# Kernel tuning notes

Hardware: AMD Instinct MI355X
Metric: run time of the kernel (lower is better)

## Reference

```python
import jax, jax.numpy as jnp
import numpy as np
from functools import partial

DN = ('NCHW', 'OIHW', 'NCHW')

def conv2d(x, w, b, stride):
    y = jax.lax.conv_general_dilated(x, w, (stride, stride), 'VALID', dimension_numbers=DN)
    return y + b[None, :, None, None]

def squash(s, eps=1e-8):
    norm = jnp.linalg.norm(s, axis=-1, keepdims=True)
    return (norm ** 2 / (1 + norm ** 2)) * s / (norm + eps)

def setup_inputs() -> dict:
    key = jax.random.key(0)
    ks = jax.random.split(key, 10)
    B, H, W = 16, 32, 512
    F, CAPS, E, OD = 64, 8, 8, 16
    H1 = (H - 6) // 2 + 1          # 14
    W1 = (W - 6) // 2 + 1          # 254
    N = F * H1 * W1 // CAPS        # 28448
    s = 0.05
    return {
        'x': jax.random.normal(ks[0], (B, H, W), jnp.float32),
        'conv1_w': jax.random.normal(ks[1], (F, 1, 6, 6), jnp.float32) * s,
        'conv1_b': jnp.zeros((F,), jnp.float32),
        'conv2_w': jax.random.normal(ks[2], (F, F, 6, 6), jnp.float32) * s,
        'conv2_b': jnp.zeros((F,), jnp.float32),
        'conv3_w': jax.random.normal(ks[3], (F, 2 * F, 1, 1), jnp.float32) * s,
        'conv3_b': jnp.zeros((F,), jnp.float32),
        'pc_w': jax.random.normal(ks[4], (N, CAPS, CAPS), jnp.float32) * s,  # [N, in, out]
        'pc_b': jnp.zeros((N, CAPS), jnp.float32),
        'ec_w': jax.random.normal(ks[5], (N, E, OD, CAPS), jnp.float32),
    }

def reference(x, conv1_w, conv1_b, conv2_w, conv2_b, conv3_w, conv3_b, pc_w, pc_b, ec_w):
    CAPS = pc_w.shape[1]
    NUM_ITER = 3
    B = x.shape[0]
    h = x[:, None]                                  # [B,1,H,W]
    h = jax.nn.relu(conv2d(h, conv1_w, conv1_b, 2)) # [B,F,14,254]
    y = jnp.pad(h, ((0, 0), (0, 0), (2, 3), (2, 3)))  # ZeroPad2d((2,3,2,3))
    y = jax.nn.relu(conv2d(y, conv2_w, conv2_b, 1))
    h = jax.nn.relu(jnp.concatenate((h, y), axis=1))
    h = conv2d(h, conv3_w, conv3_b, 1)              # [B,F,14,254]
    u_in = h.reshape(B, -1, CAPS)                   # [B,N,caps_len]
    # PrimaryCaps: N independent Linear(caps,caps) -> one batched einsum
    u = jnp.einsum('bni,nio->bno', u_in, pc_w) + pc_b[None]
    # EmotionCaps: per-capsule prediction u_hat [B,N,E,out_dim]
    u_hat = jnp.einsum('neoi,bni->bneo', ec_w, u)
    N, E = ec_w.shape[0], ec_w.shape[1]
    b_log = jnp.zeros((B, N, E), u_hat.dtype)
    v = None
    for r in range(NUM_ITER):
        c = jax.nn.softmax(b_log, axis=2)           # [B,N,E]
        s = jnp.einsum('bne,bneo->beo', c, u_hat)   # [B,E,out_dim]
        v = squash(s)
        if r < NUM_ITER - 1:
            b_log = b_log + jnp.einsum('bneo,beo->bne', u_hat, v)
    return jnp.linalg.norm(v, axis=-1)              # [B,E]
```

## Files before the change

### kernel.cpp

```cpp
#include <hip/hip_runtime.h>
#include <hip/hip_bf16.h>
#include <math.h>

#define BB 16
#define H1 14
#define W1 254
#define HPH 19
#define HPW2 264
#define NCAP 28448
#define FLATSZ 227584

typedef __attribute__((ext_vector_type(8))) short bf16x8;
typedef __attribute__((ext_vector_type(4))) float f32x4;

__device__ __forceinline__ ushort f2bf(float f) {
  __hip_bfloat16 h = __float2bfloat16(f);
  return *(ushort*)&h;
}

__global__ __launch_bounds__(256) void prep_w(const float* __restrict__ w2, const float* __restrict__ w3,
                                              ushort* __restrict__ wb, float* __restrict__ w3t) {
  int idx = blockIdx.x * 256 + threadIdx.x;
  if (idx < 147456) {
    int co = idx / 2304; int rem = idx - co * 2304;
    int tap = rem >> 6; int ci = rem & 63;
    wb[idx] = f2bf(w2[(co * 64 + ci) * 36 + tap]);
  }
  if (idx < 8192) {
    int co = idx & 63; int c = idx >> 6;
    w3t[idx] = w3[co * 128 + c];
  }
}

__global__ __launch_bounds__(256) void conv1_k(const float* __restrict__ x, const float* __restrict__ w1,
                                               const float* __restrict__ b1, float* __restrict__ hc) {
  const int i = blockIdx.x, b = blockIdx.y;
  __shared__ float xs[6 * 512];
  __shared__ float wsh[2304];
  __shared__ float bsh[64];
  const int t = threadIdx.x;
  for (int idx = t; idx < 6 * 512; idx += 256) {
    int r = idx >> 9, c = idx & 511;
    xs[idx] = x[((size_t)b * 32 + 2 * i + r) * 512 + c];
  }
  for (int idx = t; idx < 2304; idx += 256) wsh[idx] = w1[idx];
  if (t < 64) bsh[t] = b1[t];
  __syncthreads();
  if (t < 254) {
    for (int c = 0; c < 64; c++) {
      float acc = bsh[c];
#pragma unroll
      for (int p = 0; p < 6; p++)
#pragma unroll
        for (int q = 0; q < 6; q++)
          acc = fmaf(xs[p * 512 + 2 * t + q], wsh[c * 36 + p * 6 + q], acc);
      acc = fmaxf(acc, 0.f);
      hc[(((size_t)b * 64 + c) * H1 + i) * W1 + t] = acc;
    }
  }
}

__global__ __launch_bounds__(256) void nhwc_k(const float* __restrict__ hc, ushort* __restrict__ hpc) {
  const int ct = blockIdx.x, i = blockIdx.y, b = blockIdx.z;
  const int c0 = ct * 64;
  __shared__ float ls[64 * 65];
  const int t = threadIdx.x;
  for (int idx = t; idx < 4096; idx += 256) {
    int ci = idx >> 6, cc = idx & 63;
    int c = c0 + cc;
    ls[ci * 65 + cc] = (c < W1) ? hc[(((size_t)b * 64 + ci) * H1 + i) * W1 + c] : 0.f;
  }
  __syncthreads();
  uint* outp = (uint*)hpc;
  for (int idx = t; idx < 2048; idx += 256) {
    int cc = idx >> 5, ci2 = idx & 31;
    int c = c0 + cc;
    if (c < W1) {
      float f0 = ls[(2 * ci2) * 65 + cc];
      float f1 = ls[(2 * ci2 + 1) * 65 + cc];
      uint pk = (uint)f2bf(f0) | ((uint)f2bf(f1) << 16);
      outp[(((size_t)b * HPH + 2 + i) * HPW2 + 2 + c) * 32 + ci2] = pk;
    }
  }
}

__device__ __forceinline__ void stage_b(const ushort* __restrict__ wb, ushort* __restrict__ bbuf,
                                        int tap, int w, int l) {
#pragma unroll
  for (int r = 0; r < 2; r++) {
    int v = r * 256 + w * 64 + l;
    int co = v >> 3, s = v & 7;
    int g = s ^ (co & 7);
    const ushort* gp = wb + co * 2304 + tap * 64 + g * 8;
    ushort* lp = bbuf + (size_t)(r * 256 + w * 64) * 8;
    __builtin_amdgcn_global_load_lds((const uint*)gp, (uint*)lp, 16, 0, 0);
  }
}

__global__ __launch_bounds__(256, 1) void conv2_mfma(const ushort* __restrict__ hpc,
                                                     const ushort* __restrict__ wb,
                                                     const float* __restrict__ b2, float* __restrict__ y) {
  const int b = blockIdx.z, i = blockIdx.y, j0 = blockIdx.x * 128;
  const int t = threadIdx.x;
  const int w = t >> 6, l = t & 63;
  const int lr = l & 15, quad = l >> 4;

  __shared__ ushort bls[2][4096];

  f32x4 acc[2][4];
#pragma unroll
  for (int mt = 0; mt < 2; mt++)
#pragma unroll
    for (int nt = 0; nt < 4; nt++) acc[mt][nt] = (f32x4){0.f, 0.f, 0.f, 0.f};

  const ushort* abase = hpc + (((size_t)b * HPH + i) * HPW2 + (j0 + w * 32 + lr)) * 64 + quad * 8;

  bf16x8 a0[2][2], a1[2][2];

#define ALOAD(dst, tap)                                                        \
  {                                                                            \
    const int p_ = (tap) / 6, q_ = (tap) % 6;                                  \
    const ushort* ap_ = abase + ((size_t)p_ * HPW2 + q_) * 64;                 \
    dst[0][0] = *(const bf16x8*)(ap_);                                         \
    dst[0][1] = *(const bf16x8*)(ap_ + 1024);                                  \
    dst[1][0] = *(const bf16x8*)(ap_ + 32);                                    \
    dst[1][1] = *(const bf16x8*)(ap_ + 32 + 1024);                             \
  }

#define COMPUTE(a, bp)                                                         \
  {                                                                            \
    _Pragma("unroll")                                                          \
    for (int ch = 0; ch < 2; ch++) {                                           \
      const int g2 = ch * 4 + quad;                                            \
      _Pragma("unroll")                                                        \
      for (int nt = 0; nt < 4; nt++) {                                         \
        const int co = nt * 16 + lr;                                           \
        bf16x8 bf = *(const bf16x8*)((bp) + co * 64 + ((g2 ^ (co & 7)) * 8));  \
        acc[0][nt] = __builtin_amdgcn_mfma_f32_16x16x32_bf16(a[ch][0], bf, acc[0][nt], 0, 0, 0); \
        acc[1][nt] = __builtin_amdgcn_mfma_f32_16x16x32_bf16(a[ch][1], bf, acc[1][nt], 0, 0, 0); \
      }                                                                        \
    }                                                                          \
  }

  stage_b(wb, &bls[0][0], 0, w, l);
  __syncthreads();
  ALOAD(a0, 0);

  for (int tp = 0; tp < 36; tp += 2) {
    stage_b(wb, &bls[1][0], tp + 1, w, l);
    ALOAD(a1, tp + 1);
    COMPUTE(a0, &bls[0][0]);
    __syncthreads();
    if (tp + 2 < 36) {
      stage_b(wb, &bls[0][0], tp + 2, w, l);
      ALOAD(a0, tp + 2);
    }
    COMPUTE(a1, &bls[1][0]);
    __syncthreads();
  }

#pragma unroll
  for (int nt = 0; nt < 4; nt++) {
    const int co = nt * 16 + lr;
    const float bias = b2[co];
    float* yrow = y + (((size_t)b * 64 + co) * H1 + i) * W1;
#pragma unroll
    for (int mt = 0; mt < 2; mt++) {
      const int jb = j0 + w * 32 + mt * 16 + quad * 4;
#pragma unroll
      for (int r = 0; r < 4; r++) {
        int j = jb + r;
        if (j < W1) yrow[j] = fmaxf(acc[mt][nt][r] + bias, 0.f);
      }
    }
  }
#undef ALOAD
#undef COMPUTE
}

__global__ __launch_bounds__(256) void conv3_k(const float* __restrict__ hc, const float* __restrict__ y,
                                               const float* __restrict__ w3t, const float* __restrict__ b3,
                                               float* __restrict__ out3) {
  const int b = blockIdx.z, i = blockIdx.y, j0 = blockIdx.x * 64;
  __shared__ float cs[32][64];
  __shared__ float wsh[32][64];
  const int t = threadIdx.x;
  const int cog = t >> 4, jg = t & 15;
  float acc[4][4];
#pragma unroll
  for (int a = 0; a < 4; a++)
#pragma unroll
    for (int j = 0; j < 4; j++) acc[a][j] = 0.f;

  for (int ch = 0; ch < 4; ch++) {
    __syncthreads();
    for (int idx = t; idx < 2048; idx += 256) {
      int cl = idx >> 6; int j = j0 + (idx & 63);
      int c = ch * 32 + cl;
      float v = 0.f;
      if (j < W1) {
        if (c < 64) v = hc[(((size_t)b * 64 + c) * H1 + i) * W1 + j];
        else        v = y[(((size_t)b * 64 + (c - 64)) * H1 + i) * W1 + j];
      }
      cs[cl][idx & 63] = v;
    }
    for (int idx = t; idx < 2048; idx += 256)
      wsh[idx >> 6][idx & 63] = w3t[(ch * 32 + (idx >> 6)) * 64 + (idx & 63)];
    __syncthreads();
#pragma unroll
    for (int c = 0; c < 32; c++) {
      float4 xv = *(const float4*)&cs[c][jg * 4];
      float4 wv = *(const float4*)&wsh[c][cog * 4];
#pragma unroll
      for (int jj = 0; jj < 4; jj++) {
        float xx = (&xv.x)[jj];
        acc[0][jj] = fmaf(wv.x, xx, acc[0][jj]);
        acc[1][jj] = fmaf(wv.y, xx, acc[1][jj]);
        acc[2][jj] = fmaf(wv.z, xx, acc[2][jj]);
        acc[3][jj] = fmaf(wv.w, xx, acc[3][jj]);
      }
    }
  }
#pragma unroll
  for (int a = 0; a < 4; a++) {
    int co = cog * 4 + a;
    float bias = b3[co];
#pragma unroll
    for (int jj = 0; jj < 4; jj++) {
      int j = j0 + jg * 4 + jj;
      if (j < W1) out3[(((size_t)b * 64 + co) * H1 + i) * W1 + j] = acc[a][jj] + bias;
    }
  }
}

__global__ __launch_bounds__(256) void pc_k(const float* __restrict__ out3, const float* __restrict__ pcw,
                                            const float* __restrict__ pcb, float* __restrict__ u) {
  int n = blockIdx.x * 256 + threadIdx.x;
  if (n >= NCAP) return;
  float pw[64];
  const float4* pwp = (const float4*)(pcw + (size_t)n * 64);
#pragma unroll
  for (int k = 0; k < 16; k++) {
    float4 v = pwp[k];
    pw[4 * k] = v.x; pw[4 * k + 1] = v.y; pw[4 * k + 2] = v.z; pw[4 * k + 3] = v.w;
  }
  float pb[8];
  {
    const float4* pbp = (const float4*)(pcb + (size_t)n * 8);
    float4 a = pbp[0], b = pbp[1];
    pb[0] = a.x; pb[1] = a.y; pb[2] = a.z; pb[3] = a.w;
    pb[4] = b.x; pb[5] = b.y; pb[6] = b.z; pb[7] = b.w;
  }
  for (int b = 0; b < BB; b++) {
    const float4* uip = (const float4*)(out3 + (size_t)b * FLATSZ + (size_t)n * 8);
    float4 a = uip[0], c = uip[1];
    float ui[8] = {a.x, a.y, a.z, a.w, c.x, c.y, c.z, c.w};
    float uo[8];
#pragma unroll
    for (int o = 0; o < 8; o++) uo[o] = pb[o];
#pragma unroll
    for (int i2 = 0; i2 < 8; i2++)
#pragma unroll
      for (int o = 0; o < 8; o++) uo[o] = fmaf(ui[i2], pw[i2 * 8 + o], uo[o]);
    float4* up = (float4*)(u + ((size_t)b * NCAP + n) * 8);
    up[0] = make_float4(uo[0], uo[1], uo[2], uo[3]);
    up[1] = make_float4(uo[4], uo[5], uo[6], uo[7]);
  }
}

template <int MODE>
__global__ __launch_bounds__(256, 4) void route_k(const float* __restrict__ u, const float* __restrict__ ecw,
                                                  const float* __restrict__ v, float* __restrict__ sout) {
  const int t = threadIdx.x, l = t & 63, wv = t >> 6;
  const int b0 = blockIdx.y * 8;
  const int n0 = blockIdx.x * 32 + wv * 8;

  __shared__ float us[4][512];
  __shared__ float red[4096];
  __shared__ float vlds[1024];

  if (MODE) {
    for (int idx = t; idx < 1024; idx += 256) vlds[idx] = v[b0 * 128 + idx];
    __syncthreads();
  }

#pragma unroll
  for (int bb = 0; bb < 8; bb++)
    us[wv][bb * 64 + l] = u[((size_t)(b0 + bb) * NCAP + n0) * 8 + l];

  float sacc[16];
#pragma unroll
  for (int k = 0; k < 16; k++) sacc[k] = 0.f;

  for (int nn = 0; nn < 8; nn++) {
    const int n = n0 + nn;
    const float4* ep = (const float4*)(ecw + (size_t)n * 1024 + l * 16);
    float4 e0 = ep[0], e1 = ep[1], e2 = ep[2], e3 = ep[3];
    float ec[16] = {e0.x, e0.y, e0.z, e0.w, e1.x, e1.y, e1.z, e1.w,
                    e2.x, e2.y, e2.z, e2.w, e3.x, e3.y, e3.z, e3.w};
#pragma unroll
    for (int bb = 0; bb < 8; bb++) {
      const float4* up = (const float4*)&us[wv][bb * 64 + nn * 8];
      float4 ua = up[0], ubv = up[1];
      float uv[8] = {ua.x, ua.y, ua.z, ua.w, ubv.x, ubv.y, ubv.z, ubv.w};
      float h0 = 0.f, h1 = 0.f;
#pragma unroll
      for (int k = 0; k < 8; k++) { h0 = fmaf(ec[k], uv[k], h0); h1 = fmaf(ec[8 + k], uv[k], h1); }
      if (MODE == 0) {
        sacc[2 * bb] += h0; sacc[2 * bb + 1] += h1;
      } else {
        float2 vv = *(const float2*)&vlds[bb * 128 + 2 * l];
        float p = h0 * vv.x + h1 * vv.y;
        p += __shfl_xor(p, 1); p += __shfl_xor(p, 2); p += __shfl_xor(p, 4);
        float m = p;
        m = fmaxf(m, __shfl_xor(m, 8)); m = fmaxf(m, __shfl_xor(m, 16)); m = fmaxf(m, __shfl_xor(m, 32));
        float ex = __expf(p - m);
        float den = ex;
        den += __shfl_xor(den, 8); den += __shfl_xor(den, 16); den += __shfl_xor(den, 32);
        float cc = ex * __builtin_amdgcn_rcpf(den);
        sacc[2 * bb] = fmaf(cc, h0, sacc[2 * bb]);
        sacc[2 * bb + 1] = fmaf(cc, h1, sacc[2 * bb + 1]);
      }
    }
  }

#pragma unroll
  for (int k = 0; k < 16; k++) red[k * 256 + wv * 64 + l] = sacc[k];
  __syncthreads();
#pragma unroll
  for (int m = 0; m < 4; m++) {
    int slot = t + 256 * m;
    int bl = slot >> 7, eo = slot & 127;
    int k = 2 * bl + (eo & 1), l2 = eo >> 1;
    const float* r = red + k * 256 + l2;
    atomicAdd(&sout[(b0 + bl) * 128 + eo], r[0] + r[64] + r[128] + r[192]);
  }
}

__global__ void squash_k(const float* __restrict__ s, float scale, const float* __restrict__ vprev,
                         float* __restrict__ vout) {
  int t = threadIdx.x;
  const float* sp = s + t * 16;
  float sv[16]; float nn = 0.f;
#pragma unroll
  for (int o = 0; o < 16; o++) { float x = sp[o] * scale; sv[o] = x; nn = fmaf(x, x, nn); }
  float norm = sqrtf(nn);
  float f = nn / (1.f + nn) / (norm + 1e-8f);
#pragma unroll
  for (int o = 0; o < 16; o++) {
    float base = vprev ? vprev[t * 16 + o] : 0.f;
    vout[t * 16 + o] = base + f * sv[o];
  }
}

__global__ void squash_out_k(const float* __restrict__ s, float* __restrict__ out) {
  int t = threadIdx.x;
  float nn = 0.f;
#pragma unroll
  for (int o = 0; o < 16; o++) { float x = s[t * 16 + o]; nn = fmaf(x, x, nn); }
  float norm = sqrtf(nn);
  float f = nn / (1.f + nn) / (norm + 1e-8f);
  out[t] = f * norm;
}

extern "C" void kernel_launch(void* const* d_in, const int* in_sizes, int n_in,
                              void* d_out, int out_size, void* d_ws, size_t ws_size,
                              hipStream_t stream) {
  const float* x   = (const float*)d_in[0];
  const float* w1  = (const float*)d_in[1];
  const float* b1  = (const float*)d_in[2];
  const float* w2  = (const float*)d_in[3];
  const float* b2  = (const float*)d_in[4];
  const float* w3  = (const float*)d_in[5];
  const float* b3  = (const float*)d_in[6];
  const float* pcw = (const float*)d_in[7];
  const float* pcb = (const float*)d_in[8];
  const float* ecw = (const float*)d_in[9];
  float* out = (float*)d_out;

  float* ws = (float*)d_ws;
  size_t o = 0;
  float* hc   = ws + o; o += 3641344;
  float* yb   = ws + o; o += 3641344;
  float* out3 = ws + o; o += 3641344;
  ushort* hpc = (ushort*)(ws + o); o += 2568192;
  ushort* wb  = (ushort*)(ws + o); o += 73728;
  float* w3t  = ws + o; o += 8192;
  float* s0   = ws + o; o += 2048;
  float* s1   = ws + o; o += 2048;
  float* s2   = ws + o; o += 2048;
  float* v0   = ws + o; o += 2048;
  float* v1   = ws + o; o += 2048;
  float* ub   = hc;

  hipMemsetAsync(hpc, 0, (size_t)16 * HPH * HPW2 * 64 * 2, stream);
  hipMemsetAsync(s0, 0, 3 * 2048 * 4, stream);

  prep_w<<<576, 256, 0, stream>>>(w2, w3, wb, w3t);
  conv1_k<<<dim3(14, 16), 256, 0, stream>>>(x, w1, b1, hc);
  nhwc_k<<<dim3(4, 14, 16), 256, 0, stream>>>(hc, hpc);
  conv2_mfma<<<dim3(2, 14, 16), 256, 0, stream>>>(hpc, wb, b2, yb);
  conv3_k<<<dim3(4, 14, 16), 256, 0, stream>>>(hc, yb, w3t, b3, out3);
  pc_k<<<112, 256, 0, stream>>>(out3, pcw, pcb, ub);
  route_k<0><<<dim3(889, 2), 256, 0, stream>>>(ub, ecw, nullptr, s0);
  squash_k<<<1, 128, 0, stream>>>(s0, 0.125f, nullptr, v0);
  route_k<1><<<dim3(889, 2), 256, 0, stream>>>(ub, ecw, v0, s1);
  squash_k<<<1, 128, 0, stream>>>(s1, 1.0f, v0, v1);
  route_k<1><<<dim3(889, 2), 256, 0, stream>>>(ub, ecw, v1, s2);
  squash_out_k<<<1, 128, 0, stream>>>(s2, out);
}
```

Baseline: 495.6 us.

## Prefetch next capsule weights in routing kernel and drop softmax max reduction

The routing kernel now loads the ec_w row for the next capsule into registers while computing on the current one, so global loads overlap the arithmetic. The per-batch work is split into groups of four, which exposes more independent FMAs and shuffles at once. The softmax over emotions no longer subtracts the max, which removes three shuffle-max steps. The shared-memory barrier is also moved to after the u staging. Skipping the max trades numerical safety for fewer instructions, since large routing logits could overflow exp. The extra live registers may also reduce occupancy.

```diff
diff --git a/kernel.cpp b/kernel.cpp
--- a/kernel.cpp
+++ b/kernel.cpp
@@ -281,45 +281,67 @@
 
   if (MODE) {
     for (int idx = t; idx < 1024; idx += 256) vlds[idx] = v[b0 * 128 + idx];
-    __syncthreads();
-  }
-
+  }
 #pragma unroll
   for (int bb = 0; bb < 8; bb++)
     us[wv][bb * 64 + l] = u[((size_t)(b0 + bb) * NCAP + n0) * 8 + l];
+  if (MODE) __syncthreads();
 
   float sacc[16];
 #pragma unroll
   for (int k = 0; k < 16; k++) sacc[k] = 0.f;
 
+  const float4* ebase = (const float4*)(ecw + (size_t)n0 * 1024 + l * 16);
+
+  float eca[16];
+  {
+    float4 a = ebase[0], b = ebase[1], c = ebase[2], d = ebase[3];
+    eca[0]=a.x; eca[1]=a.y; eca[2]=a.z; eca[3]=a.w; eca[4]=b.x; eca[5]=b.y; eca[6]=b.z; eca[7]=b.w;
+    eca[8]=c.x; eca[9]=c.y; eca[10]=c.z; eca[11]=c.w; eca[12]=d.x; eca[13]=d.y; eca[14]=d.z; eca[15]=d.w;
+  }
+
   for (int nn = 0; nn < 8; nn++) {
-    const int n = n0 + nn;
-    const float4* ep = (const float4*)(ecw + (size_t)n * 1024 + l * 16);
-    float4 e0 = ep[0], e1 = ep[1], e2 = ep[2], e3 = ep[3];
-    float ec[16] = {e0.x, e0.y, e0.z, e0.w, e1.x, e1.y, e1.z, e1.w,
-                    e2.x, e2.y, e2.z, e2.w, e3.x, e3.y, e3.z, e3.w};
-#pragma unroll
-    for (int bb = 0; bb < 8; bb++) {
-      const float4* up = (const float4*)&us[wv][bb * 64 + nn * 8];
-      float4 ua = up[0], ubv = up[1];
-      float uv[8] = {ua.x, ua.y, ua.z, ua.w, ubv.x, ubv.y, ubv.z, ubv.w};
-      float h0 = 0.f, h1 = 0.f;
-#pragma unroll
-      for (int k = 0; k < 8; k++) { h0 = fmaf(ec[k], uv[k], h0); h1 = fmaf(ec[8 + k], uv[k], h1); }
+    float ec[16];
+#pragma unroll
+    for (int k = 0; k < 16; k++) ec[k] = eca[k];
+    if (nn < 7) {
+      const float4* ep = ebase + (nn + 1) * 256;
+      float4 a = ep[0], b = ep[1], c = ep[2], d = ep[3];
+      eca[0]=a.x; eca[1]=a.y; eca[2]=a.z; eca[3]=a.w; eca[4]=b.x; eca[5]=b.y; eca[6]=b.z; eca[7]=b.w;
+      eca[8]=c.x; eca[9]=c.y; eca[10]=c.z; eca[11]=c.w; eca[12]=d.x; eca[13]=d.y; eca[14]=d.z; eca[15]=d.w;
+    }
+#pragma unroll
+    for (int g = 0; g < 2; g++) {
+      float uh0[4], uh1[4];
+#pragma unroll
+      for (int j = 0; j < 4; j++) {
+        const float4* up = (const float4*)&us[wv][(g * 4 + j) * 64 + nn * 8];
+        float4 ua = up[0], ubv = up[1];
+        float uv[8] = {ua.x, ua.y, ua.z, ua.w, ubv.x, ubv.y, ubv.z, ubv.w};
+        float h0 = 0.f, h1 = 0.f;
+#pragma unroll
+        for (int k = 0; k < 8; k++) { h0 = fmaf(ec[k], uv[k], h0); h1 = fmaf(ec[8 + k], uv[k], h1); }
+        uh0[j] = h0; uh1[j] = h1;
+      }
       if (MODE == 0) {
-        sacc[2 * bb] += h0; sacc[2 * bb + 1] += h1;
+#pragma unroll
+        for (int j = 0; j < 4; j++) {
+          sacc[2 * (g * 4 + j)] += uh0[j]; sacc[2 * (g * 4 + j) + 1] += uh1[j];
+        }
       } else {
-        float2 vv = *(const float2*)&vlds[bb * 128 + 2 * l];
-        float p = h0 * vv.x + h1 * vv.y;
-        p += __shfl_xor(p, 1); p += __shfl_xor(p, 2); p += __shfl_xor(p, 4);
-        float m = p;
-        m = fmaxf(m, __shfl_xor(m, 8)); m = fmaxf(m, __shfl_xor(m, 16)); m = fmaxf(m, __shfl_xor(m, 32));
-        float ex = __expf(p - m);
-        float den = ex;
-        den += __shfl_xor(den, 8); den += __shfl_xor(den, 16); den += __shfl_xor(den, 32);
-        float cc = ex * __builtin_amdgcn_rcpf(den);
-        sacc[2 * bb] = fmaf(cc, h0, sacc[2 * bb]);
-        sacc[2 * bb + 1] = fmaf(cc, h1, sacc[2 * bb + 1]);
+#pragma unroll
+        for (int j = 0; j < 4; j++) {
+          const int bb = g * 4 + j;
+          float2 vv = *(const float2*)&vlds[bb * 128 + 2 * l];
+          float p = uh0[j] * vv.x + uh1[j] * vv.y;
+          p += __shfl_xor(p, 1); p += __shfl_xor(p, 2); p += __shfl_xor(p, 4);
+          float ex = __expf(p);
+          float den = ex;
+          den += __shfl_xor(den, 8); den += __shfl_xor(den, 16); den += __shfl_xor(den, 32);
+          float cc = ex * __builtin_amdgcn_rcpf(den);
+          sacc[2 * bb] = fmaf(cc, uh0[j], sacc[2 * bb]);
+          sacc[2 * bb + 1] = fmaf(cc, uh1[j], sacc[2 * bb + 1]);
+        }
       }
     }
   }
```

Result: no change. 500.8 us (+1.1%).
